# Kernel tuning notes

Measured on AMD Instinct MI355X. Metric: run time of the kernel, lower is better.

## Reference

```python
import jax, jax.numpy as jnp
import numpy as np

DIM = 512
HEADS = 16
WIN = (7, 7)
S = WIN[0] * WIN[1]          # 49 tokens per window
NW = 64                      # windows per image (mask dim)
B_IMG = 32
B = B_IMG * NW               # 2048 total windows
TABLE = (2 * WIN[0] - 1) * (2 * WIN[1] - 1)  # 169


def _relative_position_index():
    ch = np.arange(WIN[0]); cw = np.arange(WIN[1])
    coords = np.stack(np.meshgrid(ch, cw, indexing='ij')).reshape(2, -1)  # [2, S]
    rel = coords[:, :, None] - coords[:, None, :]                          # [2, S, S]
    rel = rel.transpose(1, 2, 0).astype(np.int32)
    rel[:, :, 0] += WIN[0] - 1
    rel[:, :, 1] += WIN[1] - 1
    rel[:, :, 0] *= 2 * WIN[1] - 1
    return rel.sum(-1)  # [S, S], values in [0, TABLE)


def setup_inputs() -> dict:
    key = jax.random.key(0)
    ks = jax.random.split(key, 7)
    return {
        'x': jax.random.normal(ks[0], (B, S, DIM), jnp.float32),
        'mask': jax.random.normal(ks[1], (NW, S, S), jnp.float32),
        'qkv_w': jax.random.normal(ks[2], (DIM, 3 * DIM), jnp.float32) * (DIM ** -0.5),
        'qkv_b': jax.random.normal(ks[3], (3 * DIM,), jnp.float32) * 0.02,
        'proj_w': jax.random.normal(ks[4], (DIM, DIM), jnp.float32) * (DIM ** -0.5),
        'proj_b': jax.random.normal(ks[5], (DIM,), jnp.float32) * 0.02,
        'bias_table': jax.random.normal(ks[6], (TABLE, HEADS), jnp.float32) * 0.02,
        'rel_idx': jnp.asarray(_relative_position_index()),
    }


def reference(x, mask, qkv_w, qkv_b, proj_w, proj_b, bias_table, rel_idx):
    b, s, c = x.shape
    hd = c // HEADS
    scale = hd ** -0.5
    qkv = x @ qkv_w + qkv_b                                   # [B, S, 3C]
    qkv = qkv.reshape(b, s, 3, HEADS, hd).transpose(2, 0, 3, 1, 4)
    q, k, v = qkv[0], qkv[1], qkv[2]                          # [B, H, S, hd]
    attn = jnp.einsum('bhqd,bhkd->bhqk', q * scale, k)        # [B, H, S, S]
    # gathered relative position bias: [S*S, H] -> [H, S, S]
    bias = bias_table[rel_idx.reshape(-1)].reshape(s, s, HEADS).transpose(2, 0, 1)
    attn = attn + bias[None]
    # shifted-window mask add
    nw = mask.shape[0]
    attn = attn.reshape(-1, nw, HEADS, s, s) + mask[None, :, None]
    attn = attn.reshape(-1, HEADS, s, s)
    attn = jax.nn.softmax(attn, axis=-1)
    out = jnp.einsum('bhqk,bhkd->bhqd', attn, v)              # [B, H, S, hd]
    out = out.transpose(0, 2, 1, 3).reshape(b, s, c)
    return out @ proj_w + proj_b
```

## Files before the change

kernel.cpp:

```cpp
#include <hip/hip_runtime.h>


typedef unsigned short u16;
typedef __attribute__((ext_vector_type(8))) short short8;
typedef __attribute__((ext_vector_type(4))) float floatx4;

#define B_WIN 2048
#define SEQ 49
#define DIM 512
#define NHEAD 16
#define HD 32
#define MROWS (B_WIN * SEQ)
#define QTOT 51380224u
#define VOFF 102760448u

__device__ __forceinline__ u16 f2bf(float x) {
    unsigned u = __float_as_uint(x);
    u += 0x7fffu + ((u >> 16) & 1u);
    return (u16)(u >> 16);
}

__device__ __forceinline__ void async_ld16(const void* g, void* l) {
    __builtin_amdgcn_global_load_lds(
        (const __attribute__((address_space(1))) void*)g,
        (__attribute__((address_space(3))) void*)l, 16, 0, 0);
}

__global__ void conv_f32_bf16(const float* __restrict__ in, u16* __restrict__ out, int n4) {
    int id = blockIdx.x * 256 + threadIdx.x;
    if (id >= n4) return;
    float4 v = ((const float4*)in)[id];
    uint2 o;
    o.x = (unsigned)f2bf(v.x) | ((unsigned)f2bf(v.y) << 16);
    o.y = (unsigned)f2bf(v.z) | ((unsigned)f2bf(v.w) << 16);
    *(uint2*)(out + (size_t)id * 4) = o;
}

__global__ void transpose_conv(const float* __restrict__ in, u16* __restrict__ out, int Cn) {
    int id = blockIdx.x * 256 + threadIdx.x;
    if (id >= Cn * 512) return;
    int k = id & 511;
    int n = id >> 9;
    out[id] = f2bf(in[(size_t)k * Cn + n]);
}

__global__ void build_combined(const float* __restrict__ mask, const float* __restrict__ bias_table,
                               const int* __restrict__ rel_idx, float* __restrict__ cmb) {
    int id = blockIdx.x * 256 + threadIdx.x;
    if (id >= 64 * 16 * 2401) return;
    int ij = id % 2401;
    int wh = id / 2401;
    int h = wh & 15, w = wh >> 4;
    cmb[id] = bias_table[rel_idx[ij] * NHEAD + h] + mask[(size_t)w * 2401 + ij];
}

__global__ void zero_vpad(u16* __restrict__ qkvp) {
    int id = blockIdx.x * 256 + threadIdx.x;
    if (id >= 2048 * 16 * 32) return;
    uint4 z = {0u, 0u, 0u, 0u};
    u16* p = qkvp + VOFF + (size_t)id * 64 + 48;
    *(uint4*)p = z;
    *((uint4*)p + 1) = z;
}

__global__ __launch_bounds__(256, 2)
void gemm_qkv(const u16* __restrict__ A, const u16* __restrict__ Bt,
              const float* __restrict__ bias, u16* __restrict__ qkvp) {
    const int K = 512;
    const int tid  = threadIdx.x;
    const int lane = tid & 63, wave = tid >> 6;
    const int quad = lane >> 4, l16 = lane & 15;
    const int wr = wave >> 1, wc = wave & 1;

    const int flat = blockIdx.y * 12 + blockIdx.x;
    const int swz  = (flat & 7) * 1176 + (flat >> 3);
    const int bx = swz % 12;
    const int by = swz / 12;
    const int m0 = by * 128, n0 = bx * 128;

    __shared__ u16 smem[128 * 136];
    u16* As = smem;
    u16* Bs = smem + 4096;

    const int f0 = (wave * 2 + 0) * 512 + lane * 8;
    const int f1 = (wave * 2 + 1) * 512 + lane * 8;
    const int r0 = f0 >> 5, c0 = f0 & 31;
    const int r1 = f1 >> 5, c1 = f1 & 31;
    const u16* Ab = A + (size_t)m0 * K;
    const u16* Bb = Bt + (size_t)n0 * K;

    floatx4 acc[4][4] = {};

    for (int kt = 0; kt < K; kt += 32) {
        async_ld16(Ab + (size_t)r0 * K + kt + c0, &As[f0]);
        async_ld16(Ab + (size_t)r1 * K + kt + c1, &As[f1]);
        async_ld16(Bb + (size_t)r0 * K + kt + c0, &Bs[f0]);
        async_ld16(Bb + (size_t)r1 * K + kt + c1, &Bs[f1]);
        __syncthreads();
        short8 af[4], bf[4];
#pragma unroll
        for (int i = 0; i < 4; ++i)
            af[i] = *(const short8*)&As[(wr * 64 + i * 16 + l16) * 32 + quad * 8];
#pragma unroll
        for (int j = 0; j < 4; ++j)
            bf[j] = *(const short8*)&Bs[(wc * 64 + j * 16 + l16) * 32 + quad * 8];
#pragma unroll
        for (int i = 0; i < 4; ++i)
#pragma unroll
            for (int j = 0; j < 4; ++j)
                acc[i][j] = __builtin_amdgcn_mfma_f32_16x16x32_bf16(af[i], bf[j], acc[i][j], 0, 0, 0);
        __syncthreads();
    }

#pragma unroll
    for (int j = 0; j < 4; ++j) {
        const int col = wc * 64 + j * 16 + l16;
        const float bv = bias[n0 + col];
#pragma unroll
        for (int i = 0; i < 4; ++i)
#pragma unroll
            for (int r = 0; r < 4; ++r) {
                const int row = wr * 64 + i * 16 + quad * 4 + r;
                smem[row * 136 + col] = f2bf(acc[i][j][r] + bv);
            }
    }
    __syncthreads();

    if (n0 < 1024) {
        const int c   = n0 >> 9;
        const int hh0 = (n0 & 511) >> 5;
        u16* base = qkvp + (size_t)c * QTOT;
#pragma unroll
        for (int it = 0; it < 8; ++it) {
            const int idx  = it * 256 + tid;
            const int row  = idx >> 4;
            const int hb   = (idx >> 2) & 3;
            const int part = idx & 3;
            short8 v = *(const short8*)&smem[row * 136 + hb * 32 + part * 8];
            const int rg = m0 + row;
            const int b2 = (int)((unsigned)rg / 49u);
            const int s  = rg - b2 * 49;
            *(short8*)(base + (size_t)(b2 * 16 + hh0 + hb) * 1568 + s * 32 + part * 8) = v;
        }
    } else {
        const int hh0 = (n0 - 1024) >> 5;
        u16* base = qkvp + VOFF;
#pragma unroll 16
        for (int it = 0; it < 64; ++it) {
            const int idx = it * 256 + tid;
            const int col = idx >> 7;
            const int row = idx & 127;
            const u16 v = smem[row * 136 + col];
            const int rg = m0 + row;
            const int b2 = (int)((unsigned)rg / 49u);
            const int s  = rg - b2 * 49;
            const int hh = hh0 + (col >> 5);
            const int d  = col & 31;
            base[(size_t)(b2 * 16 + hh) * 2048 + d * 64 + s] = v;
        }
    }
}

__global__ __launch_bounds__(256, 2)
void gemm_bt(const u16* __restrict__ A, const u16* __restrict__ Bt,
             const float* __restrict__ bias, float* __restrict__ Cout,
             int M, int N, int K) {
    const int tid  = threadIdx.x;
    const int lane = tid & 63, wave = tid >> 6;
    const int quad = lane >> 4, l16 = lane & 15;
    const int wr = wave >> 1, wc = wave & 1;

    const int nbx = gridDim.x, nby = gridDim.y;
    const int total = nbx * nby;
    const int flat = blockIdx.y * nbx + blockIdx.x;
    const int swz = ((total & 7) == 0) ? ((flat & 7) * (total >> 3) + (flat >> 3)) : flat;
    const int bx = swz % nbx;
    const int by = swz / nbx;
    const int m0 = by * 128, n0 = bx * 128;

    __shared__ u16 As[128 * 32];
    __shared__ u16 Bs[128 * 32];

    const int f0 = (wave * 2 + 0) * 512 + lane * 8;
    const int f1 = (wave * 2 + 1) * 512 + lane * 8;
    const int r0 = f0 >> 5, c0 = f0 & 31;
    const int r1 = f1 >> 5, c1 = f1 & 31;
    const u16* Ab = A + (size_t)m0 * K;
    const u16* Bb = Bt + (size_t)n0 * K;

    floatx4 acc[4][4] = {};

    for (int kt = 0; kt < K; kt += 32) {
        async_ld16(Ab + (size_t)r0 * K + kt + c0, &As[f0]);
        async_ld16(Ab + (size_t)r1 * K + kt + c1, &As[f1]);
        async_ld16(Bb + (size_t)r0 * K + kt + c0, &Bs[f0]);
        async_ld16(Bb + (size_t)r1 * K + kt + c1, &Bs[f1]);
        __syncthreads();
        short8 af[4], bf[4];
#pragma unroll
        for (int i = 0; i < 4; ++i)
            af[i] = *(const short8*)&As[(wr * 64 + i * 16 + l16) * 32 + quad * 8];
#pragma unroll
        for (int j = 0; j < 4; ++j)
            bf[j] = *(const short8*)&Bs[(wc * 64 + j * 16 + l16) * 32 + quad * 8];
#pragma unroll
        for (int i = 0; i < 4; ++i)
#pragma unroll
            for (int j = 0; j < 4; ++j)
                acc[i][j] = __builtin_amdgcn_mfma_f32_16x16x32_bf16(af[i], bf[j], acc[i][j], 0, 0, 0);
        __syncthreads();
    }

#pragma unroll
    for (int i = 0; i < 4; ++i) {
#pragma unroll
        for (int j = 0; j < 4; ++j) {
            int col = n0 + wc * 64 + j * 16 + l16;
            float bv = bias[col];
#pragma unroll
            for (int r = 0; r < 4; ++r) {
                int row = m0 + wr * 64 + i * 16 + quad * 4 + r;
                Cout[(size_t)row * N + col] = acc[i][j][r] + bv;
            }
        }
    }
}

__global__ __launch_bounds__(64, 4)
void attn2(const u16* __restrict__ qkvp, const float* __restrict__ cmb,
           u16* __restrict__ out) {
    const int bid = blockIdx.x;
    const int b = bid >> 4, h = bid & 15;
    const int lane = threadIdx.x;
    const int quad = lane >> 4, l16 = lane & 15;

    const u16* qb = qkvp + (size_t)(b * 16 + h) * 1568;
    const u16* kb = qb + QTOT;
    const u16* vb = qkvp + VOFF + (size_t)(b * 16 + h) * 2048;

    __shared__ u16 ps[64 * 72];

    short8 af[4], bfr[4];
#pragma unroll
    for (int i = 0; i < 4; ++i) {
        int r = i * 16 + l16; if (r > 48) r = 48;
        af[i] = *(const short8*)(qb + r * 32 + quad * 8);
    }
#pragma unroll
    for (int j = 0; j < 4; ++j) {
        int n = j * 16 + l16; if (n > 48) n = 48;
        bfr[j] = *(const short8*)(kb + n * 32 + quad * 8);
    }

    const float scale = 0.1767766952966369f;
    const float* cb = cmb + (size_t)((b & 63) * 16 + h) * 2401;

#pragma unroll
    for (int i = 0; i < 4; ++i) {
        floatx4 accS[4] = {};
#pragma unroll
        for (int j = 0; j < 4; ++j)
            accS[j] = __builtin_amdgcn_mfma_f32_16x16x32_bf16(af[i], bfr[j], accS[j], 0, 0, 0);
        const int rbase = i * 16 + quad * 4;
#pragma unroll
        for (int r = 0; r < 4; ++r) {
            int row = rbase + r;
            int rc = row < 48 ? row : 48;
            float x[4];
#pragma unroll
            for (int j = 0; j < 4; ++j) {
                int col = j * 16 + l16;
                x[j] = (col < SEQ) ? accS[j][r] * scale + cb[rc * 49 + col] : -3.0e38f;
            }
            float m = fmaxf(fmaxf(x[0], x[1]), fmaxf(x[2], x[3]));
#pragma unroll
            for (int off = 1; off < 16; off <<= 1) m = fmaxf(m, __shfl_xor(m, off));
            float e[4], s = 0.f;
#pragma unroll
            for (int j = 0; j < 4; ++j) { e[j] = __expf(x[j] - m); s += e[j]; }
#pragma unroll
            for (int off = 1; off < 16; off <<= 1) s += __shfl_xor(s, off);
            float inv = __builtin_amdgcn_rcpf(s);
#pragma unroll
            for (int j = 0; j < 4; ++j)
                ps[row * 72 + j * 16 + l16] = f2bf(e[j] * inv);
        }
    }
    __syncthreads();

    floatx4 accO[4][2] = {};
#pragma unroll
    for (int kt = 0; kt < 2; ++kt) {
        short8 pf[4], vf[2];
#pragma unroll
        for (int i = 0; i < 4; ++i)
            pf[i] = *(const short8*)&ps[(i * 16 + l16) * 72 + kt * 32 + quad * 8];
#pragma unroll
        for (int jn = 0; jn < 2; ++jn)
            vf[jn] = *(const short8*)(vb + (jn * 16 + l16) * 64 + kt * 32 + quad * 8);
#pragma unroll
        for (int i = 0; i < 4; ++i)
#pragma unroll
            for (int jn = 0; jn < 2; ++jn)
                accO[i][jn] = __builtin_amdgcn_mfma_f32_16x16x32_bf16(pf[i], vf[jn], accO[i][jn], 0, 0, 0);
    }

    u16* op = out + (size_t)b * SEQ * DIM + h * HD;
#pragma unroll
    for (int i = 0; i < 4; ++i)
#pragma unroll
        for (int jn = 0; jn < 2; ++jn)
#pragma unroll
            for (int r = 0; r < 4; ++r) {
                int row = i * 16 + quad * 4 + r;
                if (row < SEQ)
                    op[(size_t)row * DIM + jn * 16 + l16] = f2bf(accO[i][jn][r]);
            }
}

extern "C" void kernel_launch(void* const* d_in, const int* in_sizes, int n_in,
                              void* d_out, int out_size, void* d_ws, size_t ws_size,
                              hipStream_t stream) {
    const float* x         = (const float*)d_in[0];
    const float* mask      = (const float*)d_in[1];
    const float* qkv_w     = (const float*)d_in[2];
    const float* qkv_b     = (const float*)d_in[3];
    const float* proj_w    = (const float*)d_in[4];
    const float* proj_b    = (const float*)d_in[5];
    const float* bias_tab  = (const float*)d_in[6];
    const int*   rel_idx   = (const int*)d_in[7];
    float* out = (float*)d_out;

    char* ws = (char*)d_ws;
    u16*   xbf     = (u16*)(ws + 0);
    u16*   qkvp    = (u16*)(ws + 102760448);
    float* cmb     = (float*)(ws + 442499072);
    u16*   wqkv_t  = (u16*)(ws + 452333568);
    u16*   wproj_t = (u16*)(ws + 453906432);

    conv_f32_bf16<<<50176, 256, 0, stream>>>(x, xbf, 12845056);
    transpose_conv<<<3072, 256, 0, stream>>>(qkv_w, wqkv_t, 1536);
    transpose_conv<<<1024, 256, 0, stream>>>(proj_w, wproj_t, 512);
    build_combined<<<9604, 256, 0, stream>>>(mask, bias_tab, rel_idx, cmb);
    zero_vpad<<<4096, 256, 0, stream>>>(qkvp);
    gemm_qkv<<<dim3(12, 784), 256, 0, stream>>>(xbf, wqkv_t, qkv_b, qkvp);
    attn2<<<B_WIN * NHEAD, 64, 0, stream>>>(qkvp, cmb, xbf);
    gemm_bt<<<dim3(4, 784), 256, 0, stream>>>(xbf, wproj_t, proj_b, out,
                                              MROWS, 512, 512);
}
```

Baseline: 865.9 us.

## Use 256x256 tiles with 4-stage async LDS pipeline in both GEMMs

Both the QKV and projection GEMMs move from 128x128 tiles with one synchronous LDS buffer to 256x256 tiles on 8 waves. A four-slot async global-to-LDS ring keeps three K-steps in flight, with explicit vmcnt waits and a single barrier per step. LDS reads use an XOR swizzle to avoid bank conflicts, and the MFMA block runs at raised wave priority. The cost is 128KB of LDS and 128 accumulator registers per thread, which limits occupancy, and the QKV epilogue now has to scatter through shared memory in two halves.

```diff
diff --git a/kernel.cpp b/kernel.cpp
--- a/kernel.cpp
+++ b/kernel.cpp
@@ -63,165 +63,212 @@
     *((uint4*)p + 1) = z;
 }
 
-__global__ __launch_bounds__(256, 2)
+__global__ __launch_bounds__(512, 2)
 void gemm_qkv(const u16* __restrict__ A, const u16* __restrict__ Bt,
               const float* __restrict__ bias, u16* __restrict__ qkvp) {
     const int K = 512;
     const int tid  = threadIdx.x;
     const int lane = tid & 63, wave = tid >> 6;
     const int quad = lane >> 4, l16 = lane & 15;
-    const int wr = wave >> 1, wc = wave & 1;
-
-    const int flat = blockIdx.y * 12 + blockIdx.x;
-    const int swz  = (flat & 7) * 1176 + (flat >> 3);
-    const int bx = swz % 12;
-    const int by = swz / 12;
-    const int m0 = by * 128, n0 = bx * 128;
-
-    __shared__ u16 smem[128 * 136];
-    u16* As = smem;
-    u16* Bs = smem + 4096;
-
-    const int f0 = (wave * 2 + 0) * 512 + lane * 8;
-    const int f1 = (wave * 2 + 1) * 512 + lane * 8;
-    const int r0 = f0 >> 5, c0 = f0 & 31;
-    const int r1 = f1 >> 5, c1 = f1 & 31;
-    const u16* Ab = A + (size_t)m0 * K;
+    const int wr = wave >> 2, wc = wave & 3;
+
+    const int flat = blockIdx.y * 6 + blockIdx.x;
+    const int swz  = (flat & 7) * 294 + (flat >> 3);
+    const int bx = swz % 6;
+    const int by = swz / 6;
+    const int m0 = by * 256, n0 = bx * 256;
+
+    __shared__ u16 smem[65536];
+
+    const u16* Ab = A  + (size_t)m0 * K;
     const u16* Bb = Bt + (size_t)n0 * K;
 
-    floatx4 acc[4][4] = {};
-
-    for (int kt = 0; kt < K; kt += 32) {
-        async_ld16(Ab + (size_t)r0 * K + kt + c0, &As[f0]);
-        async_ld16(Ab + (size_t)r1 * K + kt + c1, &As[f1]);
-        async_ld16(Bb + (size_t)r0 * K + kt + c0, &Bs[f0]);
-        async_ld16(Bb + (size_t)r1 * K + kt + c1, &Bs[f1]);
+    const int st_row = tid >> 2;
+    const int st_chk = (((tid & 3) ^ ((tid >> 3) & 3))) * 8;
+    auto stage = [&](int t) {
+        const int slot = (t & 3) * 16384;
+        const u16* as_ = Ab + (size_t)st_row * K + t * 32 + st_chk;
+        const u16* bs_ = Bb + (size_t)st_row * K + t * 32 + st_chk;
+        async_ld16(as_,                    &smem[slot + tid * 8]);
+        async_ld16(as_ + (size_t)128 * K,  &smem[slot + 4096 + tid * 8]);
+        async_ld16(bs_,                    &smem[slot + 8192 + tid * 8]);
+        async_ld16(bs_ + (size_t)128 * K,  &smem[slot + 8192 + 4096 + tid * 8]);
+    };
+
+    floatx4 acc[8][4] = {};
+    const int qx = (quad ^ ((l16 >> 1) & 3)) * 8;
+
+    auto compute = [&](int t) {
+        const int slot = (t & 3) * 16384;
+        short8 a[8], b[4];
+#pragma unroll
+        for (int n = 0; n < 4; ++n)
+            b[n] = *(const short8*)&smem[slot + 8192 + (wc * 64 + n * 16 + l16) * 32 + qx];
+#pragma unroll
+        for (int m = 0; m < 8; ++m)
+            a[m] = *(const short8*)&smem[slot + (wr * 128 + m * 16 + l16) * 32 + qx];
+        asm volatile("s_waitcnt lgkmcnt(0)" ::: "memory");
+        __builtin_amdgcn_sched_barrier(0);
+        __builtin_amdgcn_s_setprio(1);
+#pragma unroll
+        for (int m = 0; m < 8; ++m)
+#pragma unroll
+            for (int n = 0; n < 4; ++n)
+                acc[m][n] = __builtin_amdgcn_mfma_f32_16x16x32_bf16(a[m], b[n], acc[m][n], 0, 0, 0);
+        __builtin_amdgcn_s_setprio(0);
+    };
+
+    stage(0); stage(1); stage(2);
+
+#pragma unroll 1
+    for (int t = 0; t < 14; ++t) {
+        asm volatile("s_waitcnt vmcnt(8)" ::: "memory");
+        __builtin_amdgcn_s_barrier();
+        if (t + 3 < 16) stage(t + 3);
+        compute(t);
+    }
+    asm volatile("s_waitcnt vmcnt(4)" ::: "memory");
+    __builtin_amdgcn_s_barrier();
+    compute(14);
+    asm volatile("s_waitcnt vmcnt(0)" ::: "memory");
+    __builtin_amdgcn_s_barrier();
+    compute(15);
+
+    __syncthreads();
+
+#pragma unroll 1
+    for (int h = 0; h < 2; ++h) {
+        if (wr == h) {
+#pragma unroll
+            for (int n = 0; n < 4; ++n) {
+                const int col = wc * 64 + n * 16 + l16;
+                const float bv = bias[n0 + col];
+#pragma unroll
+                for (int m = 0; m < 8; ++m)
+#pragma unroll
+                    for (int r = 0; r < 4; ++r)
+                        smem[(m * 16 + quad * 4 + r) * 264 + col] = f2bf(acc[m][n][r] + bv);
+            }
+        }
         __syncthreads();
-        short8 af[4], bf[4];
-#pragma unroll
-        for (int i = 0; i < 4; ++i)
-            af[i] = *(const short8*)&As[(wr * 64 + i * 16 + l16) * 32 + quad * 8];
-#pragma unroll
-        for (int j = 0; j < 4; ++j)
-            bf[j] = *(const short8*)&Bs[(wc * 64 + j * 16 + l16) * 32 + quad * 8];
-#pragma unroll
-        for (int i = 0; i < 4; ++i)
-#pragma unroll
-            for (int j = 0; j < 4; ++j)
-                acc[i][j] = __builtin_amdgcn_mfma_f32_16x16x32_bf16(af[i], bf[j], acc[i][j], 0, 0, 0);
+        if (n0 < 1024) {
+            const int c   = n0 >> 9;
+            const int hh0 = (n0 & 511) >> 5;
+            u16* base = qkvp + (size_t)c * QTOT;
+#pragma unroll
+            for (int it = 0; it < 8; ++it) {
+                const int idx  = it * 512 + tid;
+                const int row  = idx >> 5;
+                const int hb   = (idx >> 2) & 7;
+                const int part = idx & 3;
+                short8 v = *(const short8*)&smem[row * 264 + hb * 32 + part * 8];
+                const int rg = m0 + h * 128 + row;
+                const int b2 = (int)((unsigned)rg / 49u);
+                const int s  = rg - b2 * 49;
+                *(short8*)(base + (size_t)(b2 * 16 + hh0 + hb) * 1568 + s * 32 + part * 8) = v;
+            }
+        } else {
+            const int hh0 = (n0 - 1024) >> 5;
+            u16* base = qkvp + VOFF;
+#pragma unroll 8
+            for (int it = 0; it < 64; ++it) {
+                const int idx = it * 512 + tid;
+                const int col = idx >> 7;
+                const int row = idx & 127;
+                const u16 v = smem[row * 264 + col];
+                const int rg = m0 + h * 128 + row;
+                const int b2 = (int)((unsigned)rg / 49u);
+                const int s  = rg - b2 * 49;
+                const int hh = hh0 + (col >> 5);
+                const int d  = col & 31;
+                base[(size_t)(b2 * 16 + hh) * 2048 + d * 64 + s] = v;
+            }
+        }
         __syncthreads();
     }
-
-#pragma unroll
-    for (int j = 0; j < 4; ++j) {
-        const int col = wc * 64 + j * 16 + l16;
-        const float bv = bias[n0 + col];
-#pragma unroll
-        for (int i = 0; i < 4; ++i)
-#pragma unroll
-            for (int r = 0; r < 4; ++r) {
-                const int row = wr * 64 + i * 16 + quad * 4 + r;
-                smem[row * 136 + col] = f2bf(acc[i][j][r] + bv);
-            }
-    }
-    __syncthreads();
-
-    if (n0 < 1024) {
-        const int c   = n0 >> 9;
-        const int hh0 = (n0 & 511) >> 5;
-        u16* base = qkvp + (size_t)c * QTOT;
-#pragma unroll
-        for (int it = 0; it < 8; ++it) {
-            const int idx  = it * 256 + tid;
-            const int row  = idx >> 4;
-            const int hb   = (idx >> 2) & 3;
-            const int part = idx & 3;
-            short8 v = *(const short8*)&smem[row * 136 + hb * 32 + part * 8];
-            const int rg = m0 + row;
-            const int b2 = (int)((unsigned)rg / 49u);
-            const int s  = rg - b2 * 49;
-            *(short8*)(base + (size_t)(b2 * 16 + hh0 + hb) * 1568 + s * 32 + part * 8) = v;
-        }
-    } else {
-        const int hh0 = (n0 - 1024) >> 5;
-        u16* base = qkvp + VOFF;
-#pragma unroll 16
-        for (int it = 0; it < 64; ++it) {
-            const int idx = it * 256 + tid;
-            const int col = idx >> 7;
-            const int row = idx & 127;
-            const u16 v = smem[row * 136 + col];
-            const int rg = m0 + row;
-            const int b2 = (int)((unsigned)rg / 49u);
-            const int s  = rg - b2 * 49;
-            const int hh = hh0 + (col >> 5);
-            const int d  = col & 31;
-            base[(size_t)(b2 * 16 + hh) * 2048 + d * 64 + s] = v;
-        }
-    }
-}
-
-__global__ __launch_bounds__(256, 2)
+}
+
+__global__ __launch_bounds__(512, 2)
 void gemm_bt(const u16* __restrict__ A, const u16* __restrict__ Bt,
              const float* __restrict__ bias, float* __restrict__ Cout,
              int M, int N, int K) {
     const int tid  = threadIdx.x;
     const int lane = tid & 63, wave = tid >> 6;
     const int quad = lane >> 4, l16 = lane & 15;
-    const int wr = wave >> 1, wc = wave & 1;
-
-    const int nbx = gridDim.x, nby = gridDim.y;
-    const int total = nbx * nby;
-    const int flat = blockIdx.y * nbx + blockIdx.x;
-    const int swz = ((total & 7) == 0) ? ((flat & 7) * (total >> 3) + (flat >> 3)) : flat;
-    const int bx = swz % nbx;
-    const int by = swz / nbx;
-    const int m0 = by * 128, n0 = bx * 128;
-
-    __shared__ u16 As[128 * 32];
-    __shared__ u16 Bs[128 * 32];
-
-    const int f0 = (wave * 2 + 0) * 512 + lane * 8;
-    const int f1 = (wave * 2 + 1) * 512 + lane * 8;
-    const int r0 = f0 >> 5, c0 = f0 & 31;
-    const int r1 = f1 >> 5, c1 = f1 & 31;
-    const u16* Ab = A + (size_t)m0 * K;
+    const int wr = wave >> 2, wc = wave & 3;
+
+    const int flat = blockIdx.y * 2 + blockIdx.x;
+    const int swz  = (flat & 7) * 98 + (flat >> 3);
+    const int bx = swz & 1;
+    const int by = swz >> 1;
+    const int m0 = by * 256, n0 = bx * 256;
+
+    __shared__ u16 smem[65536];
+
+    const u16* Ab = A  + (size_t)m0 * K;
     const u16* Bb = Bt + (size_t)n0 * K;
 
-    floatx4 acc[4][4] = {};
-
-    for (int kt = 0; kt < K; kt += 32) {
-        async_ld16(Ab + (size_t)r0 * K + kt + c0, &As[f0]);
-        async_ld16(Ab + (size_t)r1 * K + kt + c1, &As[f1]);
-        async_ld16(Bb + (size_t)r0 * K + kt + c0, &Bs[f0]);
-        async_ld16(Bb + (size_t)r1 * K + kt + c1, &Bs[f1]);
-        __syncthreads();
-        short8 af[4], bf[4];
-#pragma unroll
-        for (int i = 0; i < 4; ++i)
-            af[i] = *(const short8*)&As[(wr * 64 + i * 16 + l16) * 32 + quad * 8];
-#pragma unroll
-        for (int j = 0; j < 4; ++j)
-            bf[j] = *(const short8*)&Bs[(wc * 64 + j * 16 + l16) * 32 + quad * 8];
-#pragma unroll
-        for (int i = 0; i < 4; ++i)
-#pragma unroll
-            for (int j = 0; j < 4; ++j)
-                acc[i][j] = __builtin_amdgcn_mfma_f32_16x16x32_bf16(af[i], bf[j], acc[i][j], 0, 0, 0);
-        __syncthreads();
-    }
-
-#pragma unroll
-    for (int i = 0; i < 4; ++i) {
-#pragma unroll
-        for (int j = 0; j < 4; ++j) {
-            int col = n0 + wc * 64 + j * 16 + l16;
-            float bv = bias[col];
-#pragma unroll
-            for (int r = 0; r < 4; ++r) {
-                int row = m0 + wr * 64 + i * 16 + quad * 4 + r;
-                Cout[(size_t)row * N + col] = acc[i][j][r] + bv;
-            }
+    const int st_row = tid >> 2;
+    const int st_chk = (((tid & 3) ^ ((tid >> 3) & 3))) * 8;
+    auto stage = [&](int t) {
+        const int slot = (t & 3) * 16384;
+        const u16* as_ = Ab + (size_t)st_row * K + t * 32 + st_chk;
+        const u16* bs_ = Bb + (size_t)st_row * K + t * 32 + st_chk;
+        async_ld16(as_,                    &smem[slot + tid * 8]);
+        async_ld16(as_ + (size_t)128 * K,  &smem[slot + 4096 + tid * 8]);
+        async_ld16(bs_,                    &smem[slot + 8192 + tid * 8]);
+        async_ld16(bs_ + (size_t)128 * K,  &smem[slot + 8192 + 4096 + tid * 8]);
+    };
+
+    floatx4 acc[8][4] = {};
+    const int qx = (quad ^ ((l16 >> 1) & 3)) * 8;
+
+    auto compute = [&](int t) {
+        const int slot = (t & 3) * 16384;
+        short8 a[8], b[4];
+#pragma unroll
+        for (int n = 0; n < 4; ++n)
+            b[n] = *(const short8*)&smem[slot + 8192 + (wc * 64 + n * 16 + l16) * 32 + qx];
+#pragma unroll
+        for (int m = 0; m < 8; ++m)
+            a[m] = *(const short8*)&smem[slot + (wr * 128 + m * 16 + l16) * 32 + qx];
+        asm volatile("s_waitcnt lgkmcnt(0)" ::: "memory");
+        __builtin_amdgcn_sched_barrier(0);
+        __builtin_amdgcn_s_setprio(1);
+#pragma unroll
+        for (int m = 0; m < 8; ++m)
+#pragma unroll
+            for (int n = 0; n < 4; ++n)
+                acc[m][n] = __builtin_amdgcn_mfma_f32_16x16x32_bf16(a[m], b[n], acc[m][n], 0, 0, 0);
+        __builtin_amdgcn_s_setprio(0);
+    };
+
+    stage(0); stage(1); stage(2);
+
+#pragma unroll 1
+    for (int t = 0; t < 14; ++t) {
+        asm volatile("s_waitcnt vmcnt(8)" ::: "memory");
+        __builtin_amdgcn_s_barrier();
+        if (t + 3 < 16) stage(t + 3);
+        compute(t);
+    }
+    asm volatile("s_waitcnt vmcnt(4)" ::: "memory");
+    __builtin_amdgcn_s_barrier();
+    compute(14);
+    asm volatile("s_waitcnt vmcnt(0)" ::: "memory");
+    __builtin_amdgcn_s_barrier();
+    compute(15);
+
+#pragma unroll
+    for (int n = 0; n < 4; ++n) {
+        const int col = n0 + wc * 64 + n * 16 + l16;
+        const float bv = bias[col];
+#pragma unroll
+        for (int m = 0; m < 8; ++m) {
+            const int row = m0 + wr * 128 + m * 16 + quad * 4;
+#pragma unroll
+            for (int r = 0; r < 4; ++r)
+                Cout[(size_t)(row + r) * N + col] = acc[m][n][r] + bv;
         }
     }
 }
@@ -343,8 +390,8 @@
     transpose_conv<<<1024, 256, 0, stream>>>(proj_w, wproj_t, 512);
     build_combined<<<9604, 256, 0, stream>>>(mask, bias_tab, rel_idx, cmb);
     zero_vpad<<<4096, 256, 0, stream>>>(qkvp);
-    gemm_qkv<<<dim3(12, 784), 256, 0, stream>>>(xbf, wqkv_t, qkv_b, qkvp);
+    gemm_qkv<<<dim3(6, 392), 512, 0, stream>>>(xbf, wqkv_t, qkv_b, qkvp);
     attn2<<<B_WIN * NHEAD, 64, 0, stream>>>(qkvp, cmb, xbf);
-    gemm_bt<<<dim3(4, 784), 256, 0, stream>>>(xbf, wproj_t, proj_b, out,
+    gemm_bt<<<dim3(2, 392), 512, 0, stream>>>(xbf, wproj_t, proj_b, out,
                                               MROWS, 512, 512);
 }
```

Measured after the change: 880.7 us. Within noise of the previous version (+1.7%).

## Pad combined bias/mask to 64-wide permuted rows and process two heads per block

Applied to the files above, without the earlier changes.

The precomputed bias+mask table is rebuilt with 64 padded columns in a lane-permuted order, so each lane fetches its four softmax inputs as one float4 and the padding carries a large negative value in place of per-column branches. The attention kernel now handles two heads per 64-thread block, loads Q/K fragments for both up front and prefetches V before the softmax. The table lives in the output buffer, which is free until the final projection overwrites it. This cuts scattered scalar loads and launch count, at the cost of extra barriers and more registers per block.

```diff
diff --git a/kernel.cpp b/kernel.cpp
--- a/kernel.cpp
+++ b/kernel.cpp
@@ -47,11 +47,21 @@
 __global__ void build_combined(const float* __restrict__ mask, const float* __restrict__ bias_table,
                                const int* __restrict__ rel_idx, float* __restrict__ cmb) {
     int id = blockIdx.x * 256 + threadIdx.x;
-    if (id >= 64 * 16 * 2401) return;
-    int ij = id % 2401;
-    int wh = id / 2401;
+    if (id >= 64 * 16 * 49 * 64) return;
+    int w64 = id & 63;
+    int j   = w64 & 3;
+    int l   = w64 >> 2;
+    int c   = j * 16 + l;
+    int t   = id >> 6;
+    int row = t % 49;
+    int wh  = t / 49;
     int h = wh & 15, w = wh >> 4;
-    cmb[id] = bias_table[rel_idx[ij] * NHEAD + h] + mask[(size_t)w * 2401 + ij];
+    float v = -1.0e30f;
+    if (c < 49) {
+        int ij = row * 49 + c;
+        v = bias_table[rel_idx[ij] * NHEAD + h] + mask[(size_t)w * 2401 + ij];
+    }
+    cmb[id] = v;
 }
 
 __global__ void zero_vpad(u16* __restrict__ qkvp) {
@@ -227,95 +237,112 @@
 }
 
 __global__ __launch_bounds__(64, 4)
-void attn2(const u16* __restrict__ qkvp, const float* __restrict__ cmb,
+void attn2(const u16* __restrict__ qkvp, const float* __restrict__ cmbp,
            u16* __restrict__ out) {
-    const int bid = blockIdx.x;
-    const int b = bid >> 4, h = bid & 15;
     const int lane = threadIdx.x;
     const int quad = lane >> 4, l16 = lane & 15;
-
-    const u16* qb = qkvp + (size_t)(b * 16 + h) * 1568;
-    const u16* kb = qb + QTOT;
-    const u16* vb = qkvp + VOFF + (size_t)(b * 16 + h) * 2048;
+    const int p0 = blockIdx.x * 2;
+    const int b  = p0 >> 4, h0 = p0 & 15;
+
+    const u16* qb0 = qkvp + (size_t)p0 * 1568;
+    const u16* kb0 = qb0 + QTOT;
+    const u16* qb1 = qb0 + 1568;
+    const u16* kb1 = kb0 + 1568;
+    const u16* vb0 = qkvp + VOFF + (size_t)p0 * 2048;
+    const u16* vb1 = vb0 + 2048;
+
+    const float* cb0 = cmbp + (size_t)(((b & 63) * 16 + h0) * 49) * 64;
+    const float* cb1 = cb0 + 49 * 64;
+
+    u16* op0 = out + (size_t)b * SEQ * DIM + h0 * HD;
+    u16* op1 = op0 + HD;
 
     __shared__ u16 ps[64 * 72];
 
-    short8 af[4], bfr[4];
-#pragma unroll
-    for (int i = 0; i < 4; ++i) {
-        int r = i * 16 + l16; if (r > 48) r = 48;
-        af[i] = *(const short8*)(qb + r * 32 + quad * 8);
-    }
-#pragma unroll
-    for (int j = 0; j < 4; ++j) {
-        int n = j * 16 + l16; if (n > 48) n = 48;
-        bfr[j] = *(const short8*)(kb + n * 32 + quad * 8);
-    }
+    int rr[4];
+#pragma unroll
+    for (int i = 0; i < 4; ++i) { int r = i * 16 + l16; rr[i] = r > 48 ? 48 : r; }
+
+    short8 af0[4], bf0[4], af1[4], bf1[4];
+#pragma unroll
+    for (int i = 0; i < 4; ++i) af0[i] = *(const short8*)(qb0 + rr[i] * 32 + quad * 8);
+#pragma unroll
+    for (int j = 0; j < 4; ++j) bf0[j] = *(const short8*)(kb0 + rr[j] * 32 + quad * 8);
+#pragma unroll
+    for (int i = 0; i < 4; ++i) af1[i] = *(const short8*)(qb1 + rr[i] * 32 + quad * 8);
+#pragma unroll
+    for (int j = 0; j < 4; ++j) bf1[j] = *(const short8*)(kb1 + rr[j] * 32 + quad * 8);
 
     const float scale = 0.1767766952966369f;
-    const float* cb = cmb + (size_t)((b & 63) * 16 + h) * 2401;
-
-#pragma unroll
-    for (int i = 0; i < 4; ++i) {
-        floatx4 accS[4] = {};
-#pragma unroll
-        for (int j = 0; j < 4; ++j)
-            accS[j] = __builtin_amdgcn_mfma_f32_16x16x32_bf16(af[i], bfr[j], accS[j], 0, 0, 0);
-        const int rbase = i * 16 + quad * 4;
-#pragma unroll
-        for (int r = 0; r < 4; ++r) {
-            int row = rbase + r;
-            int rc = row < 48 ? row : 48;
-            float x[4];
-#pragma unroll
-            for (int j = 0; j < 4; ++j) {
-                int col = j * 16 + l16;
-                x[j] = (col < SEQ) ? accS[j][r] * scale + cb[rc * 49 + col] : -3.0e38f;
+
+    auto do_pair = [&](const short8* af, const short8* bfr, const float* cb,
+                       const u16* vb, u16* op) {
+        short8 vf[2][2];
+#pragma unroll
+        for (int kt = 0; kt < 2; ++kt)
+#pragma unroll
+            for (int jn = 0; jn < 2; ++jn)
+                vf[kt][jn] = *(const short8*)(vb + (jn * 16 + l16) * 64 + kt * 32 + quad * 8);
+
+#pragma unroll
+        for (int i = 0; i < 4; ++i) {
+            floatx4 accS[4] = {};
+#pragma unroll
+            for (int j = 0; j < 4; ++j)
+                accS[j] = __builtin_amdgcn_mfma_f32_16x16x32_bf16(af[i], bfr[j], accS[j], 0, 0, 0);
+            const int rbase = i * 16 + quad * 4;
+#pragma unroll
+            for (int r = 0; r < 4; ++r) {
+                const int row = rbase + r;
+                const int rc = row < 48 ? row : 48;
+                float4 c4 = *(const float4*)(cb + rc * 64 + l16 * 4);
+                float x[4] = { accS[0][r] * scale + c4.x, accS[1][r] * scale + c4.y,
+                               accS[2][r] * scale + c4.z, accS[3][r] * scale + c4.w };
+                float m = fmaxf(fmaxf(x[0], x[1]), fmaxf(x[2], x[3]));
+#pragma unroll
+                for (int off = 1; off < 16; off <<= 1) m = fmaxf(m, __shfl_xor(m, off));
+                float e[4], s = 0.f;
+#pragma unroll
+                for (int j = 0; j < 4; ++j) { e[j] = __expf(x[j] - m); s += e[j]; }
+#pragma unroll
+                for (int off = 1; off < 16; off <<= 1) s += __shfl_xor(s, off);
+                float inv = __builtin_amdgcn_rcpf(s);
+#pragma unroll
+                for (int j = 0; j < 4; ++j)
+                    ps[row * 72 + j * 16 + l16] = f2bf(e[j] * inv);
             }
-            float m = fmaxf(fmaxf(x[0], x[1]), fmaxf(x[2], x[3]));
-#pragma unroll
-            for (int off = 1; off < 16; off <<= 1) m = fmaxf(m, __shfl_xor(m, off));
-            float e[4], s = 0.f;
-#pragma unroll
-            for (int j = 0; j < 4; ++j) { e[j] = __expf(x[j] - m); s += e[j]; }
-#pragma unroll
-            for (int off = 1; off < 16; off <<= 1) s += __shfl_xor(s, off);
-            float inv = __builtin_amdgcn_rcpf(s);
-#pragma unroll
-            for (int j = 0; j < 4; ++j)
-                ps[row * 72 + j * 16 + l16] = f2bf(e[j] * inv);
-        }
-    }
-    __syncthreads();
-
-    floatx4 accO[4][2] = {};
-#pragma unroll
-    for (int kt = 0; kt < 2; ++kt) {
-        short8 pf[4], vf[2];
-#pragma unroll
-        for (int i = 0; i < 4; ++i)
-            pf[i] = *(const short8*)&ps[(i * 16 + l16) * 72 + kt * 32 + quad * 8];
-#pragma unroll
-        for (int jn = 0; jn < 2; ++jn)
-            vf[jn] = *(const short8*)(vb + (jn * 16 + l16) * 64 + kt * 32 + quad * 8);
+        }
+        __syncthreads();
+
+        floatx4 accO[4][2] = {};
+#pragma unroll
+        for (int kt = 0; kt < 2; ++kt) {
+            short8 pf[4];
+#pragma unroll
+            for (int i = 0; i < 4; ++i)
+                pf[i] = *(const short8*)&ps[(i * 16 + l16) * 72 + kt * 32 + quad * 8];
+#pragma unroll
+            for (int i = 0; i < 4; ++i)
+#pragma unroll
+                for (int jn = 0; jn < 2; ++jn)
+                    accO[i][jn] = __builtin_amdgcn_mfma_f32_16x16x32_bf16(pf[i], vf[kt][jn], accO[i][jn], 0, 0, 0);
+        }
+        __syncthreads();
+
 #pragma unroll
         for (int i = 0; i < 4; ++i)
 #pragma unroll
             for (int jn = 0; jn < 2; ++jn)
-                accO[i][jn] = __builtin_amdgcn_mfma_f32_16x16x32_bf16(pf[i], vf[jn], accO[i][jn], 0, 0, 0);
-    }
-
-    u16* op = out + (size_t)b * SEQ * DIM + h * HD;
-#pragma unroll
-    for (int i = 0; i < 4; ++i)
-#pragma unroll
-        for (int jn = 0; jn < 2; ++jn)
-#pragma unroll
-            for (int r = 0; r < 4; ++r) {
-                int row = i * 16 + quad * 4 + r;
-                if (row < SEQ)
-                    op[(size_t)row * DIM + jn * 16 + l16] = f2bf(accO[i][jn][r]);
-            }
+#pragma unroll
+                for (int r = 0; r < 4; ++r) {
+                    int row = i * 16 + quad * 4 + r;
+                    if (row < SEQ)
+                        op[(size_t)row * DIM + jn * 16 + l16] = f2bf(accO[i][jn][r]);
+                }
+    };
+
+    do_pair(af0, bf0, cb0, vb0, op0);
+    do_pair(af1, bf1, cb1, vb1, op1);
 }
 
 extern "C" void kernel_launch(void* const* d_in, const int* in_sizes, int n_in,
@@ -334,17 +361,17 @@
     char* ws = (char*)d_ws;
     u16*   xbf     = (u16*)(ws + 0);
     u16*   qkvp    = (u16*)(ws + 102760448);
-    float* cmb     = (float*)(ws + 442499072);
     u16*   wqkv_t  = (u16*)(ws + 452333568);
     u16*   wproj_t = (u16*)(ws + 453906432);
+    float* cmb     = out;
 
     conv_f32_bf16<<<50176, 256, 0, stream>>>(x, xbf, 12845056);
     transpose_conv<<<3072, 256, 0, stream>>>(qkv_w, wqkv_t, 1536);
     transpose_conv<<<1024, 256, 0, stream>>>(proj_w, wproj_t, 512);
-    build_combined<<<9604, 256, 0, stream>>>(mask, bias_tab, rel_idx, cmb);
+    build_combined<<<12544, 256, 0, stream>>>(mask, bias_tab, rel_idx, cmb);
     zero_vpad<<<4096, 256, 0, stream>>>(qkvp);
     gemm_qkv<<<dim3(12, 784), 256, 0, stream>>>(xbf, wqkv_t, qkv_b, qkvp);
-    attn2<<<B_WIN * NHEAD, 64, 0, stream>>>(qkvp, cmb, xbf);
+    attn2<<<B_WIN * NHEAD / 2, 64, 0, stream>>>(qkvp, cmb, xbf);
     gemm_bt<<<dim3(4, 784), 256, 0, stream>>>(xbf, wproj_t, proj_b, out,
                                               MROWS, 512, 512);
 }
```

New measurement: 856.2 us. No clear change (-1.1%).
